# Kernel optimization log

Measured on AMD Instinct MI355X. Metric: run time of the kernel, lower is better.

Reference implementation:

```python
import jax, jax.numpy as jnp
import numpy as np

B, H, W, DIM, HEADS, WS, SHIFT = 16, 64, 64, 512, 16, 8, 4
HEAD_DIM = DIM // HEADS
MLP_HID = 4 * DIM
N_WIN = (H // WS) * (W // WS)
NW = WS * WS  # tokens per window
SCALE = HEAD_DIM ** -0.5
LN_EPS = 1e-5


def _np_win_partition(x, ws):
    # replicates rearrange 'b (s1 h2) (s2 w2) c -> (b h2 w2) (s1 s2) c' (interleaved partition)
    b, h, w, c = x.shape
    h2, w2 = h // ws, w // ws
    x = x.reshape(b, ws, h2, ws, w2, c).transpose(0, 2, 4, 1, 3, 5)
    return x.reshape(b * h2 * w2, ws * ws, c)


def _build_mask():
    img = np.zeros((1, H, W, 1), np.float32)
    sl = [slice(0, -WS), slice(-WS, -SHIFT), slice(-SHIFT, None)]
    cnt = 0
    for hs in sl:
        for ws_ in sl:
            img[:, hs, ws_, :] = cnt
            cnt += 1
    wm = _np_win_partition(img, WS).reshape(-1, NW)  # (N_WIN, NW)
    diff = wm[:, None, :] - wm[:, :, None]
    mask = np.where(diff == 0, 1.0, 0.0).astype(np.float32)
    return (1.0 - mask) * -1e10  # (N_WIN, NW, NW) additive mask


def _rel_index():
    ch = np.arange(WS)
    coords = np.stack(np.meshgrid(ch, ch, indexing='ij')).reshape(2, -1)  # (2, NW)
    rel = (coords[:, :, None] - coords[:, None, :]).transpose(1, 2, 0)  # (NW, NW, 2)
    rel[..., 0] += WS - 1
    rel[..., 1] += WS - 1
    rel[..., 0] *= 2 * WS - 1
    return rel.sum(-1)  # (NW, NW) int


MASK = jnp.asarray(_build_mask())
REL_IDX = jnp.asarray(_rel_index().reshape(-1))


def _win_partition(x):  # (B, H, W, C) -> (B*N_WIN, NW, C)
    h2, w2 = H // WS, W // WS
    x = x.reshape(B, WS, h2, WS, w2, DIM).transpose(0, 2, 4, 1, 3, 5)
    return x.reshape(B * h2 * w2, WS * WS, DIM)


def _win_reverse(w):  # (B*N_WIN, NW, C) -> (B, H*W, C), inverse of the interleaved partition
    h2, w2 = H // WS, W // WS
    x = w.reshape(B, h2, w2, WS, WS, DIM).transpose(0, 3, 1, 4, 2, 5)
    return x.reshape(B, H * W, DIM)


def _ln(x, w, b):
    m = x.mean(-1, keepdims=True)
    v = jnp.mean((x - m) ** 2, axis=-1, keepdims=True)
    return (x - m) / jnp.sqrt(v + LN_EPS) * w + b


def setup_inputs() -> dict:
    key = jax.random.key(0)
    ks = jax.random.split(key, 6)
    std = 0.02
    return {
        'x': jax.random.normal(ks[0], (B, H * W, DIM), jnp.float32),
        'ln1_w': jnp.ones((DIM,), jnp.float32),
        'ln1_b': jnp.zeros((DIM,), jnp.float32),
        'qkv_w': jax.random.normal(ks[1], (3 * DIM, DIM), jnp.float32) * std,
        'qkv_b': jnp.zeros((3 * DIM,), jnp.float32),
        'rpb_table': jax.random.normal(ks[2], ((2 * WS - 1) ** 2, HEADS), jnp.float32) * std,
        'proj_w': jax.random.normal(ks[3], (DIM, DIM), jnp.float32) * std,
        'proj_b': jnp.zeros((DIM,), jnp.float32),
        'ln2_w': jnp.ones((DIM,), jnp.float32),
        'ln2_b': jnp.zeros((DIM,), jnp.float32),
        'fc1_w': jax.random.normal(ks[4], (MLP_HID, DIM), jnp.float32) * std,
        'fc1_b': jnp.zeros((MLP_HID,), jnp.float32),
        'fc2_w': jax.random.normal(ks[5], (DIM, MLP_HID), jnp.float32) * std,
        'fc2_b': jnp.zeros((DIM,), jnp.float32),
    }


def reference(x, ln1_w, ln1_b, qkv_w, qkv_b, rpb_table, proj_w, proj_b,
              ln2_w, ln2_b, fc1_w, fc1_b, fc2_w, fc2_b):
    h = x
    y = _ln(x, ln1_w, ln1_b).reshape(B, H, W, DIM)
    y = jnp.roll(y, (-SHIFT, -SHIFT), axis=(1, 2))  # cyclic shift
    xw = _win_partition(y)  # (B*N_WIN, NW, DIM)

    qkv = xw @ qkv_w.T + qkv_b  # (B*N_WIN, NW, 3*DIM)
    # original splits channel as (heads, head_dim, qkv) with qkv innermost
    qkv = qkv.reshape(B * N_WIN, NW, HEADS, HEAD_DIM, 3)
    q = qkv[..., 0].transpose(0, 2, 1, 3) * SCALE  # (Bw, H, NW, d)
    k = qkv[..., 1].transpose(0, 2, 1, 3)
    v = qkv[..., 2].transpose(0, 2, 1, 3)

    attn = jnp.einsum('bhqd,bhkd->bhqk', q, k)
    bias = rpb_table[REL_IDX].reshape(NW, NW, HEADS).transpose(2, 0, 1)  # (H, NW, NW)
    attn = attn + bias[None]
    # shift mask: per-window additive mask broadcast over batch and heads
    attn = attn.reshape(B, N_WIN, HEADS, NW, NW) + MASK[None, :, None]
    attn = jax.nn.softmax(attn, axis=-1).reshape(B * N_WIN, HEADS, NW, NW)

    out = jnp.einsum('bhqk,bhkd->bhqd', attn, v)
    out = out.transpose(0, 2, 1, 3).reshape(B * N_WIN, NW, DIM)
    out = out @ proj_w.T + proj_b

    attn_out = _win_reverse(out)  # (B, H*W, DIM)
    # NOTE: faithful to original - attention output is NOT rolled back before residual
    x2 = h + attn_out

    z = _ln(x2, ln2_w, ln2_b)
    z = jax.nn.gelu(z @ fc1_w.T + fc1_b, approximate=False)
    z = z @ fc2_w.T + fc2_b
    return x2 + z
```

## Files before the change

kernel.cpp:

```cpp
#include <hip/hip_runtime.h>
#include <math.h>

typedef short short8 __attribute__((ext_vector_type(8)));
typedef float f32x4 __attribute__((ext_vector_type(4)));
typedef unsigned short u16;
typedef u16 us4 __attribute__((ext_vector_type(4)));

#define DEVI static __device__ __forceinline__

constexpr float SCALE_Q = 0.17677669529663687f;

DEVI u16 f2bf(float f) {
  unsigned u = __builtin_bit_cast(unsigned, f);
  u += 0x7FFFu + ((u >> 16) & 1u);
  return (u16)(u >> 16);
}

DEVI float gelu_t(float val) {
  float u = val * (0.79788456f + 0.03567740814f * val * val);
  float e = __expf(2.f * u);
  return val * (1.f - __builtin_amdgcn_rcpf(e + 1.f));
}

DEVI void gload16(const u16* g, u16* l) {
  __builtin_amdgcn_global_load_lds((const __attribute__((address_space(1))) void*)g,
                                   (__attribute__((address_space(3))) void*)l,
                                   16, 0, 0);
}

DEVI short8 ldsw(const u16* base, int r, int g) {
  return *(const short8*)(base + r * 32 + (((g + (r >> 1)) & 3) << 3));
}

__global__ void cvt_bf16(const float4* __restrict__ src, us4* __restrict__ dst, int n4) {
  int i = blockIdx.x * 256 + threadIdx.x;
  if (i < n4) {
    float4 v = src[i];
    us4 o = { f2bf(v.x), f2bf(v.y), f2bf(v.z), f2bf(v.w) };
    dst[i] = o;
  }
}

__global__ void cvt_qkvw(const float4* __restrict__ src, us4* __restrict__ dst) {
  int i = blockIdx.x * 256 + threadIdx.x;
  int row = i >> 7, c4 = i & 127;
  int which = row >> 9, head = (row >> 5) & 15, d = row & 31;
  int srow = head * 96 + d * 3 + which;
  float4 v = src[srow * 128 + c4];
  us4 o = { f2bf(v.x), f2bf(v.y), f2bf(v.z), f2bf(v.w) };
  dst[i] = o;
}

__global__ void perm_qkvb(const float* __restrict__ src, float* __restrict__ dst) {
  int i = blockIdx.x * 256 + threadIdx.x;
  int which = i >> 9, head = (i >> 5) & 15, d = i & 31;
  dst[i] = src[head * 96 + d * 3 + which];
}

template<bool PERM>
__global__ __launch_bounds__(256) void ln_kernel(const float* __restrict__ src,
                                                 const float* __restrict__ gw,
                                                 const float* __restrict__ gb,
                                                 u16* __restrict__ dst) {
  int wid = threadIdx.x >> 6, lane = threadIdx.x & 63;
  int m = blockIdx.x * 4 + wid;
  int srow;
  if (PERM) {
    int b = m >> 12;
    int win = (m >> 6) & 63, t = m & 63;
    int i2 = win >> 3, j2 = win & 7, s1 = t >> 3, s2 = t & 7;
    int h = (s1 * 8 + i2 + 4) & 63, w = (s2 * 8 + j2 + 4) & 63;
    srow = (b << 12) + h * 64 + w;
  } else {
    srow = m;
  }
  const float4* r4 = (const float4*)(src + (size_t)srow * 512);
  float4 v0 = r4[lane], v1 = r4[lane + 64];
  float s  = v0.x + v0.y + v0.z + v0.w + v1.x + v1.y + v1.z + v1.w;
  float ss = v0.x*v0.x + v0.y*v0.y + v0.z*v0.z + v0.w*v0.w
           + v1.x*v1.x + v1.y*v1.y + v1.z*v1.z + v1.w*v1.w;
  #pragma unroll
  for (int off = 1; off < 64; off <<= 1) {
    s  += __shfl_xor(s, off);
    ss += __shfl_xor(ss, off);
  }
  float mean = s * (1.f/512.f);
  float var  = ss * (1.f/512.f) - mean*mean;
  float rstd = rsqrtf(var + 1e-5f);
  const float4* w4 = (const float4*)gw;
  const float4* b4 = (const float4*)gb;
  float4 wa = w4[lane], ba = b4[lane], wb = w4[lane+64], bb = b4[lane+64];
  us4 o0 = { f2bf((v0.x-mean)*rstd*wa.x + ba.x),
             f2bf((v0.y-mean)*rstd*wa.y + ba.y),
             f2bf((v0.z-mean)*rstd*wa.z + ba.z),
             f2bf((v0.w-mean)*rstd*wa.w + ba.w) };
  us4 o1 = { f2bf((v1.x-mean)*rstd*wb.x + bb.x),
             f2bf((v1.y-mean)*rstd*wb.y + bb.y),
             f2bf((v1.z-mean)*rstd*wb.z + bb.z),
             f2bf((v1.w-mean)*rstd*wb.w + bb.w) };
  us4* d4 = (us4*)(dst + (size_t)m * 512);
  d4[lane] = o0; d4[lane + 64] = o1;
}

template<int MODE, int NT>
__global__ __launch_bounds__(256, 4) void gemm_k(const u16* __restrict__ A,
                                                 const u16* __restrict__ Bw,
                                                 const float* __restrict__ bias,
                                                 u16* __restrict__ o0, u16* __restrict__ o1,
                                                 u16* __restrict__ o2,
                                                 float* __restrict__ fo,
                                                 const float* __restrict__ resid,
                                                 int M, int N) {
  const int K = NT * 32;
  __shared__ u16 LDS[3][2][4096];
  int nt = N >> 7;
  int nwg = gridDim.x, cpx = nwg >> 3, bid = blockIdx.x;
  int swz = (bid & 7) * cpx + (bid >> 3);
  int tm = swz / nt, tn = swz % nt;
  int tid = threadIdx.x, lane = tid & 63, wv = tid >> 6;
  int wm = wv >> 1, wn = wv & 1;
  int rr = lane & 15, g = lane >> 4;

  int srow = tid >> 2;
  int sch = (((tid & 3) - (srow >> 1)) & 3) << 3;
  const u16* a0 = A  + (size_t)(tm * 128 + srow) * K + sch;
  const u16* b0 = Bw + (size_t)(tn * 128 + srow) * K + sch;
  size_t k64 = (size_t)64 * K;

#define STG(buf, kt) { \
    u16* dA = &LDS[buf][0][0] + (wv << 9); u16* dB = &LDS[buf][1][0] + (wv << 9); \
    gload16(a0 + (kt) * 32, dA); gload16(a0 + k64 + (kt) * 32, dA + 2048); \
    gload16(b0 + (kt) * 32, dB); gload16(b0 + k64 + (kt) * 32, dB + 2048); }

  f32x4 acc[4][4] = {};

  STG(0, 0); STG(1, 1);
  asm volatile("s_waitcnt vmcnt(4)" ::: "memory");
  __builtin_amdgcn_s_barrier();

  #pragma unroll
  for (int kt = 0; kt < NT; ++kt) {
    const int cur = kt % 3;
    const int nb = (kt + 2) % 3;
    if (kt + 2 < NT) STG(nb, kt + 2);
    const u16* AT = &LDS[cur][0][0];
    const u16* BT = &LDS[cur][1][0];
    short8 af[4], bf[4];
    #pragma unroll
    for (int mi = 0; mi < 4; mi++) af[mi] = ldsw(AT, wm*64 + mi*16 + rr, g);
    #pragma unroll
    for (int ni = 0; ni < 4; ni++) bf[ni] = ldsw(BT, wn*64 + ni*16 + rr, g);
    __builtin_amdgcn_s_setprio(1);
    #pragma unroll
    for (int mi = 0; mi < 4; mi++)
      #pragma unroll
      for (int ni = 0; ni < 4; ni++)
        acc[mi][ni] = __builtin_amdgcn_mfma_f32_16x16x32_bf16(af[mi], bf[ni], acc[mi][ni], 0, 0, 0);
    __builtin_amdgcn_s_setprio(0);
    if (kt + 2 < NT) { asm volatile("s_waitcnt vmcnt(4)" ::: "memory"); }
    else             { asm volatile("s_waitcnt vmcnt(0)" ::: "memory"); }
    __builtin_amdgcn_s_barrier();
  }
#undef STG

  __syncthreads();
  u16* wreg = &LDS[0][0][0] + wv * 4096;
  int rb0 = tm * 128 + wm * 64;
  int cb0 = tn * 128 + wn * 64;

  if (MODE == 0) {
    bool isV = (tn >= 8);
    if (!isV) {
      #pragma unroll
      for (int mi = 0; mi < 4; mi++)
        #pragma unroll
        for (int ni = 0; ni < 4; ni++) {
          float bv = bias[cb0 + ni * 16 + rr];
          #pragma unroll
          for (int r = 0; r < 4; r++) {
            float val = acc[mi][ni][r] + bv;
            if (tn < 4) val *= SCALE_Q;
            int row = mi * 16 + g * 4 + r;
            int col = ni * 16 + rr;
            wreg[row * 64 + (((col >> 3) ^ (row & 7)) << 3) + (col & 7)] = f2bf(val);
          }
        }
      int row = lane;
      #pragma unroll
      for (int chk = 0; chk < 8; chk++) {
        short8 vd = *(const short8*)&wreg[row * 64 + ((chk ^ (row & 7)) << 3)];
        int grow = rb0 + row;
        int w = grow >> 6, tt = grow & 63;
        int colp = (tn & 3) * 128 + wn * 64 + chk * 8;
        int head = colp >> 5;
        u16* dst = (tn < 4) ? o0 : o1;
        *(short8*)(dst + ((size_t)(w * 16 + head) * 64 + tt) * 32 + (colp & 31)) = vd;
      }
    } else {
      #pragma unroll
      for (int mi = 0; mi < 4; mi++)
        #pragma unroll
        for (int ni = 0; ni < 4; ni++) {
          float bv = bias[cb0 + ni * 16 + rr];
          #pragma unroll
          for (int r = 0; r < 4; r++) {
            float val = acc[mi][ni][r] + bv;
            int row = mi * 16 + g * 4 + r;
            int col = ni * 16 + rr;
            wreg[col * 64 + (((row >> 3) ^ (col & 7)) << 3) + (row & 7)] = f2bf(val);
          }
        }
      int cb0v = cb0 - 1024;
      int col = lane;
      int head = (cb0v + col) >> 5, d = (cb0v + col) & 31;
      int w = rb0 >> 6;
      #pragma unroll
      for (int chk = 0; chk < 8; chk++) {
        short8 vd = *(const short8*)&wreg[col * 64 + ((chk ^ (col & 7)) << 3)];
        *(short8*)(o2 + ((size_t)(w * 16 + head) * 32 + d) * 64 + chk * 8) = vd;
      }
    }
  } else {
    #pragma unroll
    for (int ni = 0; ni < 4; ni++) {
      int col = cb0 + ni * 16 + rr;
      float bv = bias[col];
      #pragma unroll
      for (int mi = 0; mi < 4; mi++) {
        #pragma unroll
        for (int r = 0; r < 4; r++) {
          int row = rb0 + mi * 16 + g * 4 + r;
          float val = acc[mi][ni][r] + bv;
          int w = row >> 6, t = row & 63;
          int b = w >> 6, win = w & 63;
          int i2 = win >> 3, j2 = win & 7, s1 = t >> 3, s2 = t & 7;
          int pos = (b << 12) + (s1 * 8 + i2) * 64 + (s2 * 8 + j2);
          size_t idx = (size_t)pos * 512 + col;
          fo[idx] = resid[idx] + val;
        }
      }
    }
  }
}

__global__ __launch_bounds__(512, 2) void fused_mlp(const u16* __restrict__ z,
                                                    const u16* __restrict__ W1,
                                                    const u16* __restrict__ W2,
                                                    const float* __restrict__ b1,
                                                    const float* __restrict__ b2,
                                                    float* __restrict__ out) {
  __shared__ u16 As[32768];
  __shared__ u16 Hb[2][16384];
  int tid = threadIdx.x, lane = tid & 63, wv = tid >> 6;
  int rr = lane & 15, g = lane >> 4;
  int m0 = blockIdx.x * 64;

  #pragma unroll
  for (int l = 0; l < 8; l++) {
    int L = l * 512 + tid;
    int r = L >> 6, sck = L & 63;
    gload16(z + (size_t)(m0 + r) * 512 + ((sck ^ (r & 7)) << 3), &As[L * 8]);
  }
  asm volatile("s_waitcnt vmcnt(0)" ::: "memory");
  __builtin_amdgcn_s_barrier();

  f32x4 acc2[4][4] = {};

  #pragma unroll 2
  for (int c = 0; c < 8; ++c) {
    u16* H = &Hb[c & 1][0];
    f32x4 acc1[4][2] = {};
    int cb1 = c * 256 + wv * 32;
    #pragma unroll
    for (int st = 0; st < 16; ++st) {
      short8 bf1[2], af1[4];
      #pragma unroll
      for (int ni = 0; ni < 2; ni++)
        bf1[ni] = *(const short8*)(W1 + (size_t)(cb1 + ni * 16 + rr) * 512 + st * 32 + g * 8);
      #pragma unroll
      for (int mi = 0; mi < 4; mi++) {
        int row = mi * 16 + rr;
        af1[mi] = *(const short8*)(&As[row * 512 + (((st * 4 + g) ^ (row & 7)) << 3)]);
      }
      #pragma unroll
      for (int mi = 0; mi < 4; mi++)
        #pragma unroll
        for (int ni = 0; ni < 2; ni++)
          acc1[mi][ni] = __builtin_amdgcn_mfma_f32_16x16x32_bf16(af1[mi], bf1[ni], acc1[mi][ni], 0, 0, 0);
    }
    #pragma unroll
    for (int ni = 0; ni < 2; ni++) {
      int colg = wv * 32 + ni * 16 + rr;
      float bv = b1[c * 256 + colg];
      #pragma unroll
      for (int mi = 0; mi < 4; mi++)
        #pragma unroll
        for (int q = 0; q < 4; q++) {
          int row = mi * 16 + g * 4 + q;
          float val = gelu_t(acc1[mi][ni][q] + bv);
          H[row * 256 + (((colg >> 3) ^ (row & 7)) << 3) + (colg & 7)] = f2bf(val);
        }
    }
    __syncthreads();
    #pragma unroll
    for (int st = 0; st < 8; ++st) {
      short8 wb[4], ha[4];
      #pragma unroll
      for (int ni = 0; ni < 4; ni++)
        wb[ni] = *(const short8*)(W2 + (size_t)(wv * 64 + ni * 16 + rr) * 2048 + c * 256 + st * 32 + g * 8);
      #pragma unroll
      for (int mi = 0; mi < 4; mi++) {
        int row = mi * 16 + rr;
        ha[mi] = *(const short8*)(&H[row * 256 + (((st * 4 + g) ^ (row & 7)) << 3)]);
      }
      __builtin_amdgcn_s_setprio(1);
      #pragma unroll
      for (int mi = 0; mi < 4; mi++)
        #pragma unroll
        for (int ni = 0; ni < 4; ni++)
          acc2[mi][ni] = __builtin_amdgcn_mfma_f32_16x16x32_bf16(ha[mi], wb[ni], acc2[mi][ni], 0, 0, 0);
      __builtin_amdgcn_s_setprio(0);
    }
  }

  #pragma unroll
  for (int ni = 0; ni < 4; ni++) {
    int col = wv * 64 + ni * 16 + rr;
    float bv = b2[col];
    #pragma unroll
    for (int mi = 0; mi < 4; mi++)
      #pragma unroll
      for (int q = 0; q < 4; q++) {
        size_t idx = (size_t)(m0 + mi * 16 + g * 4 + q) * 512 + col;
        out[idx] += acc2[mi][ni][q] + bv;
      }
  }
}

DEVI int zone1(int x) { return x < 56 ? 0 : (x < 60 ? 1 : 2); }

__global__ __launch_bounds__(256) void attn_k(const u16* __restrict__ qb,
                                              const u16* __restrict__ kb,
                                              const u16* __restrict__ vtb,
                                              const float* __restrict__ rpb,
                                              u16* __restrict__ outb) {
  __shared__ u16 P[4][64][72];
  int wid = threadIdx.x >> 6, lane = threadIdx.x & 63;
  int p = blockIdx.x * 4 + wid;
  int w = p >> 4, head = p & 15;
  const u16* qq = qb  + (size_t)p * 2048;
  const u16* kk = kb  + (size_t)p * 2048;
  const u16* vv = vtb + (size_t)p * 2048;
  int rr = lane & 15, g = lane >> 4;

  short8 qf[4], kf[4];
  #pragma unroll
  for (int i = 0; i < 4; i++) qf[i] = *(const short8*)(qq + (i*16 + rr)*32 + g*8);
  #pragma unroll
  for (int i = 0; i < 4; i++) kf[i] = *(const short8*)(kk + (i*16 + rr)*32 + g*8);

  f32x4 zero = {0.f, 0.f, 0.f, 0.f};
  f32x4 s[4][4];
  #pragma unroll
  for (int qi = 0; qi < 4; qi++)
    #pragma unroll
    for (int kj = 0; kj < 4; kj++)
      s[qi][kj] = __builtin_amdgcn_mfma_f32_16x16x32_bf16(qf[qi], kf[kj], zero, 0, 0, 0);

  int win = w & 63, i2 = win >> 3, j2 = win & 7;
  #pragma unroll
  for (int qi = 0; qi < 4; qi++) {
    #pragma unroll
    for (int r = 0; r < 4; r++) {
      int i = qi*16 + g*4 + r;
      int s1i = i >> 3, s2i = i & 7;
      int zi = zone1(s1i*8 + i2)*3 + zone1(s2i*8 + j2);
      #pragma unroll
      for (int kj = 0; kj < 4; kj++) {
        int j = kj*16 + rr;
        int s1j = j >> 3, s2j = j & 7;
        float bv = rpb[((s1i - s1j + 7)*15 + (s2i - s2j + 7))*16 + head];
        int zj = zone1(s1j*8 + i2)*3 + zone1(s2j*8 + j2);
        s[qi][kj][r] += bv + (zi != zj ? -1e10f : 0.f);
      }
    }
  }

  float inv[4][4];
  #pragma unroll
  for (int qi = 0; qi < 4; qi++) {
    #pragma unroll
    for (int r = 0; r < 4; r++) {
      float mx = fmaxf(fmaxf(s[qi][0][r], s[qi][1][r]), fmaxf(s[qi][2][r], s[qi][3][r]));
      mx = fmaxf(mx, __shfl_xor(mx, 1));
      mx = fmaxf(mx, __shfl_xor(mx, 2));
      mx = fmaxf(mx, __shfl_xor(mx, 4));
      mx = fmaxf(mx, __shfl_xor(mx, 8));
      float sum = 0.f;
      #pragma unroll
      for (int kj = 0; kj < 4; kj++) {
        float e = __expf(s[qi][kj][r] - mx);
        s[qi][kj][r] = e;
        sum += e;
      }
      sum += __shfl_xor(sum, 1);
      sum += __shfl_xor(sum, 2);
      sum += __shfl_xor(sum, 4);
      sum += __shfl_xor(sum, 8);
      inv[qi][r] = 1.f / sum;
    }
  }

  #pragma unroll
  for (int qi = 0; qi < 4; qi++)
    #pragma unroll
    for (int kj = 0; kj < 4; kj++)
      #pragma unroll
      for (int r = 0; r < 4; r++)
        P[wid][qi*16 + g*4 + r][kj*16 + rr] = f2bf(s[qi][kj][r]);

  f32x4 o[4][2] = {};
  #pragma unroll
  for (int jh = 0; jh < 2; jh++) {
    short8 vf[2];
    #pragma unroll
    for (int df = 0; df < 2; df++)
      vf[df] = *(const short8*)(vv + (size_t)(df*16 + rr)*64 + jh*32 + g*8);
    #pragma unroll
    for (int qi = 0; qi < 4; qi++) {
      short8 pf = *(const short8*)(&P[wid][qi*16 + rr][jh*32 + g*8]);
      #pragma unroll
      for (int df = 0; df < 2; df++)
        o[qi][df] = __builtin_amdgcn_mfma_f32_16x16x32_bf16(pf, vf[df], o[qi][df], 0, 0, 0);
    }
  }

  #pragma unroll
  for (int qi = 0; qi < 4; qi++)
    #pragma unroll
    for (int df = 0; df < 2; df++)
      #pragma unroll
      for (int r = 0; r < 4; r++) {
        int t = qi*16 + g*4 + r;
        int d = df*16 + rr;
        outb[(size_t)(w*64 + t)*512 + head*32 + d] = f2bf(o[qi][df][r] * inv[qi][r]);
      }
}

extern "C" void kernel_launch(void* const* d_in, const int* in_sizes, int n_in,
                              void* d_out, int out_size, void* d_ws, size_t ws_size,
                              hipStream_t stream) {
  const float* x     = (const float*)d_in[0];
  const float* ln1w  = (const float*)d_in[1];
  const float* ln1b  = (const float*)d_in[2];
  const float* qkvw  = (const float*)d_in[3];
  const float* qkvb  = (const float*)d_in[4];
  const float* rpb   = (const float*)d_in[5];
  const float* projw = (const float*)d_in[6];
  const float* projb = (const float*)d_in[7];
  const float* ln2w  = (const float*)d_in[8];
  const float* ln2b  = (const float*)d_in[9];
  const float* fc1w  = (const float*)d_in[10];
  const float* fc1b  = (const float*)d_in[11];
  const float* fc2w  = (const float*)d_in[12];
  const float* fc2b  = (const float*)d_in[13];
  float* out = (float*)d_out;

  char* ws = (char*)d_ws;
  u16* wqkv  = (u16*)(ws + 0);
  u16* wproj = (u16*)(ws + 1572864);
  u16* wfc1  = (u16*)(ws + 2097152);
  u16* wfc2  = (u16*)(ws + 4194304);
  float* pb  = (float*)(ws + 6291456);
  size_t base = 8ull << 20;
  u16* xw = (u16*)(ws + base);
  u16* qb = (u16*)(ws + base + (64ull  << 20));
  u16* kb = (u16*)(ws + base + (128ull << 20));
  u16* vb = (u16*)(ws + base + (192ull << 20));
  u16* attnb = xw;
  u16* zb    = xw;

  cvt_qkvw<<<768, 256, 0, stream>>>((const float4*)qkvw, (us4*)wqkv);
  perm_qkvb<<<6, 256, 0, stream>>>(qkvb, pb);
  cvt_bf16<<<256,  256, 0, stream>>>((const float4*)projw, (us4*)wproj, 65536);
  cvt_bf16<<<1024, 256, 0, stream>>>((const float4*)fc1w,  (us4*)wfc1,  262144);
  cvt_bf16<<<1024, 256, 0, stream>>>((const float4*)fc2w,  (us4*)wfc2,  262144);

  ln_kernel<true><<<16384, 256, 0, stream>>>(x, ln1w, ln1b, xw);
  gemm_k<0, 16><<<6144, 256, 0, stream>>>(xw, wqkv, pb, qb, kb, vb, nullptr, nullptr,
                                          65536, 1536);
  attn_k<<<4096, 256, 0, stream>>>(qb, kb, vb, rpb, attnb);
  gemm_k<1, 16><<<2048, 256, 0, stream>>>(attnb, wproj, projb, nullptr, nullptr, nullptr,
                                          out, x, 65536, 512);
  ln_kernel<false><<<16384, 256, 0, stream>>>(out, ln2w, ln2b, zb);
  fused_mlp<<<1024, 512, 0, stream>>>(zb, wfc1, wfc2, fc1b, fc2b, out);
}
```

Measured before the change: 984.7 us.

## Shrink MLP hidden chunk to 128 and single-buffer H to raise occupancy

The fused MLP kernel now processes the hidden dimension in 16 chunks of 128 instead of 8 chunks of 256. It uses a single 16KB H buffer in place of the double-buffered 64KB one, and asks for 4 blocks per CU instead of 2. The smaller LDS and register footprint is meant to let more waves hide the latency of the global weight loads. In exchange it adds an extra barrier per chunk and loses the overlap the double buffer gave. It also caps registers harder, which risks spills with the 64-float acc2 accumulator.

```diff
diff --git a/kernel.cpp b/kernel.cpp
--- a/kernel.cpp
+++ b/kernel.cpp
@@ -243,14 +243,14 @@
   }
 }
 
-__global__ __launch_bounds__(512, 2) void fused_mlp(const u16* __restrict__ z,
+__global__ __launch_bounds__(512, 4) void fused_mlp(const u16* __restrict__ z,
                                                     const u16* __restrict__ W1,
                                                     const u16* __restrict__ W2,
                                                     const float* __restrict__ b1,
                                                     const float* __restrict__ b2,
                                                     float* __restrict__ out) {
   __shared__ u16 As[32768];
-  __shared__ u16 Hb[2][16384];
+  __shared__ u16 H[8192];
   int tid = threadIdx.x, lane = tid & 63, wv = tid >> 6;
   int rr = lane & 15, g = lane >> 4;
   int m0 = blockIdx.x * 64;
@@ -265,61 +265,62 @@
   __builtin_amdgcn_s_barrier();
 
   f32x4 acc2[4][4] = {};
-
-  #pragma unroll 2
-  for (int c = 0; c < 8; ++c) {
-    u16* H = &Hb[c & 1][0];
-    f32x4 acc1[4][2] = {};
-    int cb1 = c * 256 + wv * 32;
+  const u16* w1base = W1 + (size_t)(wv * 16 + rr) * 512 + g * 8;
+  const u16* w2base = W2 + (size_t)(wv * 64 + rr) * 2048 + g * 8;
+
+  for (int c = 0; c < 16; ++c) {
+    f32x4 acc1[4] = {};
+    const u16* w1p = w1base + (size_t)c * 128 * 512;
     #pragma unroll
     for (int st = 0; st < 16; ++st) {
-      short8 bf1[2], af1[4];
-      #pragma unroll
-      for (int ni = 0; ni < 2; ni++)
-        bf1[ni] = *(const short8*)(W1 + (size_t)(cb1 + ni * 16 + rr) * 512 + st * 32 + g * 8);
+      short8 wb1 = *(const short8*)(w1p + st * 32);
+      short8 af[4];
       #pragma unroll
       for (int mi = 0; mi < 4; mi++) {
         int row = mi * 16 + rr;
-        af1[mi] = *(const short8*)(&As[row * 512 + (((st * 4 + g) ^ (row & 7)) << 3)]);
-      }
+        af[mi] = *(const short8*)(&As[row * 512 + (((st * 4 + g) ^ (row & 7)) << 3)]);
+      }
+      __builtin_amdgcn_s_setprio(1);
       #pragma unroll
       for (int mi = 0; mi < 4; mi++)
-        #pragma unroll
-        for (int ni = 0; ni < 2; ni++)
-          acc1[mi][ni] = __builtin_amdgcn_mfma_f32_16x16x32_bf16(af1[mi], bf1[ni], acc1[mi][ni], 0, 0, 0);
-    }
-    #pragma unroll
-    for (int ni = 0; ni < 2; ni++) {
-      int colg = wv * 32 + ni * 16 + rr;
-      float bv = b1[c * 256 + colg];
+        acc1[mi] = __builtin_amdgcn_mfma_f32_16x16x32_bf16(af[mi], wb1, acc1[mi], 0, 0, 0);
+      __builtin_amdgcn_s_setprio(0);
+    }
+    __syncthreads();
+    {
+      int colg = wv * 16 + rr;
+      float bv = b1[c * 128 + colg];
+      int cc = colg >> 3, cw = colg & 7;
       #pragma unroll
       for (int mi = 0; mi < 4; mi++)
         #pragma unroll
         for (int q = 0; q < 4; q++) {
           int row = mi * 16 + g * 4 + q;
-          float val = gelu_t(acc1[mi][ni][q] + bv);
-          H[row * 256 + (((colg >> 3) ^ (row & 7)) << 3) + (colg & 7)] = f2bf(val);
+          H[row * 128 + ((cc ^ (row & 7)) << 3) + cw] = f2bf(gelu_t(acc1[mi][q] + bv));
         }
     }
     __syncthreads();
-    #pragma unroll
-    for (int st = 0; st < 8; ++st) {
-      short8 wb[4], ha[4];
-      #pragma unroll
-      for (int ni = 0; ni < 4; ni++)
-        wb[ni] = *(const short8*)(W2 + (size_t)(wv * 64 + ni * 16 + rr) * 2048 + c * 256 + st * 32 + g * 8);
+    const u16* w2p = w2base + c * 128;
+    #pragma unroll
+    for (int st2 = 0; st2 < 4; ++st2) {
+      short8 ha[4];
       #pragma unroll
       for (int mi = 0; mi < 4; mi++) {
         int row = mi * 16 + rr;
-        ha[mi] = *(const short8*)(&H[row * 256 + (((st * 4 + g) ^ (row & 7)) << 3)]);
-      }
-      __builtin_amdgcn_s_setprio(1);
-      #pragma unroll
-      for (int mi = 0; mi < 4; mi++)
+        ha[mi] = *(const short8*)(&H[row * 128 + (((st2 * 4 + g) ^ (row & 7)) << 3)]);
+      }
+      #pragma unroll
+      for (int nip = 0; nip < 2; nip++) {
+        short8 wb2a = *(const short8*)(w2p + (size_t)(nip * 32) * 2048 + st2 * 32);
+        short8 wb2b = *(const short8*)(w2p + (size_t)(nip * 32 + 16) * 2048 + st2 * 32);
+        __builtin_amdgcn_s_setprio(1);
         #pragma unroll
-        for (int ni = 0; ni < 4; ni++)
-          acc2[mi][ni] = __builtin_amdgcn_mfma_f32_16x16x32_bf16(ha[mi], wb[ni], acc2[mi][ni], 0, 0, 0);
-      __builtin_amdgcn_s_setprio(0);
+        for (int mi = 0; mi < 4; mi++) {
+          acc2[mi][nip*2]   = __builtin_amdgcn_mfma_f32_16x16x32_bf16(ha[mi], wb2a, acc2[mi][nip*2], 0, 0, 0);
+          acc2[mi][nip*2+1] = __builtin_amdgcn_mfma_f32_16x16x32_bf16(ha[mi], wb2b, acc2[mi][nip*2+1], 0, 0, 0);
+        }
+        __builtin_amdgcn_s_setprio(0);
+      }
     }
   }
 
```

After: 1.125 ms. 1.14x slower.
